# Kernel tuning notes

Hardware: AMD Instinct MI355X
Metric: run time of the kernel (lower is better)

## Reference

```python
import jax, jax.numpy as jnp
import numpy as np

N_NODES = 100000
N_EDGES = 3200000
IN_C, HID_C, OUT_C = 64, 64, 32


def setup_inputs() -> dict:
    key = jax.random.key(0)
    ks = jax.random.split(key, 8)
    x = jax.random.normal(ks[0], (N_NODES, IN_C), dtype=jnp.float32)
    edge_index = jax.random.randint(ks[1], (2, N_EDGES), 0, N_NODES, dtype=jnp.int64)
    s1 = 1.0 / np.sqrt(IN_C)
    s2 = 1.0 / np.sqrt(HID_C)
    W1l = jax.random.uniform(ks[2], (IN_C, HID_C), jnp.float32, -s1, s1)
    b1l = jnp.zeros((HID_C,), jnp.float32)
    W1r = jax.random.uniform(ks[3], (IN_C, HID_C), jnp.float32, -s1, s1)
    W2l = jax.random.uniform(ks[4], (HID_C, OUT_C), jnp.float32, -s2, s2)
    b2l = jnp.zeros((OUT_C,), jnp.float32)
    W2r = jax.random.uniform(ks[5], (HID_C, OUT_C), jnp.float32, -s2, s2)
    return {"x": x, "edge_index": edge_index, "W1l": W1l, "b1l": b1l,
            "W1r": W1r, "W2l": W2l, "b2l": b2l, "W2r": W2r}


def _sage_conv(x, src, dst, Wl, bl, Wr):
    # mean-aggregate source features onto destination nodes
    msg = x[src]                                              # [E, d] gather
    summed = jax.ops.segment_sum(msg, dst, num_segments=N_NODES)
    deg = jax.ops.segment_sum(jnp.ones((src.shape[0],), x.dtype), dst,
                              num_segments=N_NODES)
    agg = summed / jnp.maximum(deg, 1.0)[:, None]             # [N, d]
    return agg @ Wl + bl + x @ Wr                             # lin_l(agg)+lin_r(x)


def reference(x, edge_index, W1l, b1l, W1r, W2l, b2l, W2r):
    src, dst = edge_index[0], edge_index[1]
    h = jax.nn.relu(_sage_conv(x, src, dst, W1l, b1l, W1r))
    # dropout is identity in eval mode
    return _sage_conv(h, src, dst, W2l, b2l, W2r)
```

## Files before the change

kernel.cpp:

```cpp
#include <hip/hip_runtime.h>
#include <hip/hip_bf16.h>

#define N_NODES 100000
#define N_EDGES 3200000
#define NBKT 391
#define BKT_CAP 10240

typedef __hip_bfloat16 bf16;
typedef unsigned int uint;
typedef __attribute__((ext_vector_type(8))) short bf16x8;
typedef __attribute__((ext_vector_type(4))) float f32x4;

__device__ __forceinline__ float b2f(bf16 v) { return __bfloat162float(v); }

__device__ __forceinline__ float bits2f(unsigned short w) {
    union { unsigned short u; bf16 b; } c;
    c.u = w;
    return __bfloat162float(c.b);
}
__device__ __forceinline__ unsigned short f2bits(float f) {
    return (unsigned short)(__float_as_uint(f) >> 16);
}
__device__ __forceinline__ unsigned short f2bf_bits(float f) {
    bf16 b = __float2bfloat16(f);
    unsigned short u;
    __builtin_memcpy(&u, &b, 2);
    return u;
}

__device__ __forceinline__ int get_idx(const void* ei, long long pos, int is64) {
    if (is64) return (int)((const long long*)ei)[pos];
    return ((const int*)ei)[pos];
}
__device__ __forceinline__ float get_f(const void* p, long long pos, int isbf) {
    if (isbf) return b2f(((const bf16*)p)[pos]);
    return ((const float*)p)[pos];
}

__global__ void detect_kernel(const void* __restrict__ x,
                              const void* __restrict__ ei,
                              int* __restrict__ flags) {
    int lane = threadIdx.x;
    const unsigned short* xw = (const unsigned short*)x;
    float v = bits2f(xw[2 * lane]);
    bool plaus = (v == v) && fabsf(v) > 1e-3f && fabsf(v) < 1e2f;
    unsigned long long m1 = __ballot(plaus);
    const int* iw = (const int*)ei;
    bool z = (iw[2 * lane + 1] == 0);
    unsigned long long m2 = __ballot(z);
    if (lane == 0) {
        flags[0] = (__popcll(m1) >= 32) ? 1 : 0;
        flags[1] = (__popcll(m2) == 64) ? 1 : 0;
    }
}

__global__ __launch_bounds__(256) void scatterA_kernel(
    const void* __restrict__ ei, int* __restrict__ bucket_cursor,
    uint* __restrict__ bucket_data, const int* __restrict__ flags) {
    __shared__ int lhist[NBKT];
    __shared__ int lbase[NBKT];
    int is64 = flags[1];
    int t = threadIdx.x;
    int chunk0 = blockIdx.x * 8192;
    int dreg[32];

    for (int i = t; i < NBKT; i += 256) lhist[i] = 0;
    __syncthreads();
#pragma unroll
    for (int j = 0; j < 32; j++) {
        int e = chunk0 + j * 256 + t;
        int d = -1;
        if (e < N_EDGES) {
            d = get_idx(ei, (long long)N_EDGES + e, is64);
            atomicAdd(&lhist[d >> 8], 1);
        }
        dreg[j] = d;
    }
    __syncthreads();
    for (int i = t; i < NBKT; i += 256) {
        int c = lhist[i];
        lbase[i] = c ? atomicAdd(&bucket_cursor[i], c) : 0;
        lhist[i] = 0;
    }
    __syncthreads();
#pragma unroll
    for (int j = 0; j < 32; j++) {
        int e = chunk0 + j * 256 + t;
        int d = dreg[j];
        if (d >= 0) {
            int s = get_idx(ei, e, is64);
            int b = d >> 8;
            int o = lbase[b] + atomicAdd(&lhist[b], 1);
            if (o < BKT_CAP)
                bucket_data[(long long)b * BKT_CAP + o] = ((uint)(d & 255) << 17) | (uint)s;
        }
    }
}

__global__ void scanBuckets_kernel(const int* __restrict__ cnt,
                                   int* __restrict__ base) {
    __shared__ int buf[512];
    int t = threadIdx.x;
    int v = (t < NBKT) ? cnt[t] : 0;
    buf[t] = v;
    __syncthreads();
    for (int off = 1; off < 512; off <<= 1) {
        int add = (t >= off) ? buf[t - off] : 0;
        __syncthreads();
        buf[t] += add;
        __syncthreads();
    }
    if (t < NBKT) base[t] = buf[t] - v;
}

__global__ __launch_bounds__(256) void csrB_kernel(
    const int* __restrict__ bucket_cnt, const int* __restrict__ bucket_base,
    const uint* __restrict__ bucket_data, int* __restrict__ csr_src,
    int* __restrict__ row_start) {
    __shared__ int lh[256];
    __shared__ int buf[256];
    int b = blockIdx.x;
    int t = threadIdx.x;
    int cnt = bucket_cnt[b];
    if (cnt > BKT_CAP) cnt = BKT_CAP;
    int base = bucket_base[b];
    const uint* bd = bucket_data + (long long)b * BKT_CAP;

    lh[t] = 0;
    __syncthreads();
    for (int i = t; i < cnt; i += 256) atomicAdd(&lh[bd[i] >> 17], 1);
    __syncthreads();
    int v = lh[t];
    buf[t] = v;
    __syncthreads();
    for (int off = 1; off < 256; off <<= 1) {
        int add = (t >= off) ? buf[t - off] : 0;
        __syncthreads();
        buf[t] += add;
        __syncthreads();
    }
    int excl = buf[t] - v;
    int g = (b << 8) + t;
    if (g < N_NODES) row_start[g] = base + excl;
    lh[t] = excl;
    __syncthreads();
    for (int i = t; i < cnt; i += 256) {
        uint e = bd[i];
        int o = atomicAdd(&lh[e >> 17], 1);
        csr_src[base + o] = (int)(e & 0x1FFFFu);
    }
    if (b == 0 && t == 0) row_start[N_NODES] = N_EDGES;
}

__global__ __launch_bounds__(256) void gather1_kernel(
    const void* __restrict__ x, const int* __restrict__ row_start,
    const int* __restrict__ csr_src, bf16* __restrict__ aggbuf,
    const int* __restrict__ flags) {
    int isbf = flags[0];
    int t = threadIdx.x;
    int lane = t & 63;
    int gw = (blockIdx.x * 256 + t) >> 6;
    int nw = (gridDim.x * 256) >> 6;
    int e8 = lane >> 3, q8 = lane & 7;
    int e4 = lane >> 4, q16 = lane & 15;
    const uint4* xr4 = (const uint4*)x;

    for (int p = gw; p * 2 < N_NODES; p += nw) {
        int na = p * 2, nb = p * 2 + 1;
        int sa = row_start[na], ea = row_start[na + 1];
        int sb = row_start[nb], eb = row_start[nb + 1];
        int da = ea - sa, db = eb - sb;
        int maxd = max(da, db);
        float accA[8] = {0, 0, 0, 0, 0, 0, 0, 0};
        float accB[8] = {0, 0, 0, 0, 0, 0, 0, 0};
        float avA = 0.0f, avB = 0.0f;
        if (isbf) {
            for (int off = 0; off < maxd; off += 32) {
                int iA0 = sa + off + e8, iA1 = iA0 + 8, iA2 = iA0 + 16, iA3 = iA0 + 24;
                int iB0 = sb + off + e8, iB1 = iB0 + 8, iB2 = iB0 + 16, iB3 = iB0 + 24;
                int sA0 = (iA0 < ea) ? csr_src[iA0] : -1;
                int sA1 = (iA1 < ea) ? csr_src[iA1] : -1;
                int sA2 = (iA2 < ea) ? csr_src[iA2] : -1;
                int sA3 = (iA3 < ea) ? csr_src[iA3] : -1;
                int sB0 = (iB0 < eb) ? csr_src[iB0] : -1;
                int sB1 = (iB1 < eb) ? csr_src[iB1] : -1;
                int sB2 = (iB2 < eb) ? csr_src[iB2] : -1;
                int sB3 = (iB3 < eb) ? csr_src[iB3] : -1;
                uint4 vA0 = {0,0,0,0}, vA1 = {0,0,0,0}, vA2 = {0,0,0,0}, vA3 = {0,0,0,0};
                uint4 vB0 = {0,0,0,0}, vB1 = {0,0,0,0}, vB2 = {0,0,0,0}, vB3 = {0,0,0,0};
                if (sA0 >= 0) vA0 = xr4[sA0 * 8 + q8];
                if (sA1 >= 0) vA1 = xr4[sA1 * 8 + q8];
                if (sA2 >= 0) vA2 = xr4[sA2 * 8 + q8];
                if (sA3 >= 0) vA3 = xr4[sA3 * 8 + q8];
                if (sB0 >= 0) vB0 = xr4[sB0 * 8 + q8];
                if (sB1 >= 0) vB1 = xr4[sB1 * 8 + q8];
                if (sB2 >= 0) vB2 = xr4[sB2 * 8 + q8];
                if (sB3 >= 0) vB3 = xr4[sB3 * 8 + q8];
                accA[0] += __uint_as_float(vA0.x << 16) + __uint_as_float(vA1.x << 16)
                         + __uint_as_float(vA2.x << 16) + __uint_as_float(vA3.x << 16);
                accA[1] += __uint_as_float(vA0.x & 0xffff0000u) + __uint_as_float(vA1.x & 0xffff0000u)
                         + __uint_as_float(vA2.x & 0xffff0000u) + __uint_as_float(vA3.x & 0xffff0000u);
                accA[2] += __uint_as_float(vA0.y << 16) + __uint_as_float(vA1.y << 16)
                         + __uint_as_float(vA2.y << 16) + __uint_as_float(vA3.y << 16);
                accA[3] += __uint_as_float(vA0.y & 0xffff0000u) + __uint_as_float(vA1.y & 0xffff0000u)
                         + __uint_as_float(vA2.y & 0xffff0000u) + __uint_as_float(vA3.y & 0xffff0000u);
                accA[4] += __uint_as_float(vA0.z << 16) + __uint_as_float(vA1.z << 16)
                         + __uint_as_float(vA2.z << 16) + __uint_as_float(vA3.z << 16);
                accA[5] += __uint_as_float(vA0.z & 0xffff0000u) + __uint_as_float(vA1.z & 0xffff0000u)
                         + __uint_as_float(vA2.z & 0xffff0000u) + __uint_as_float(vA3.z & 0xffff0000u);
                accA[6] += __uint_as_float(vA0.w << 16) + __uint_as_float(vA1.w << 16)
                         + __uint_as_float(vA2.w << 16) + __uint_as_float(vA3.w << 16);
                accA[7] += __uint_as_float(vA0.w & 0xffff0000u) + __uint_as_float(vA1.w & 0xffff0000u)
                         + __uint_as_float(vA2.w & 0xffff0000u) + __uint_as_float(vA3.w & 0xffff0000u);
                accB[0] += __uint_as_float(vB0.x << 16) + __uint_as_float(vB1.x << 16)
                         + __uint_as_float(vB2.x << 16) + __uint_as_float(vB3.x << 16);
                accB[1] += __uint_as_float(vB0.x & 0xffff0000u) + __uint_as_float(vB1.x & 0xffff0000u)
                         + __uint_as_float(vB2.x & 0xffff0000u) + __uint_as_float(vB3.x & 0xffff0000u);
                accB[2] += __uint_as_float(vB0.y << 16) + __uint_as_float(vB1.y << 16)
                         + __uint_as_float(vB2.y << 16) + __uint_as_float(vB3.y << 16);
                accB[3] += __uint_as_float(vB0.y & 0xffff0000u) + __uint_as_float(vB1.y & 0xffff0000u)
                         + __uint_as_float(vB2.y & 0xffff0000u) + __uint_as_float(vB3.y & 0xffff0000u);
                accB[4] += __uint_as_float(vB0.z << 16) + __uint_as_float(vB1.z << 16)
                         + __uint_as_float(vB2.z << 16) + __uint_as_float(vB3.z << 16);
                accB[5] += __uint_as_float(vB0.z & 0xffff0000u) + __uint_as_float(vB1.z & 0xffff0000u)
                         + __uint_as_float(vB2.z & 0xffff0000u) + __uint_as_float(vB3.z & 0xffff0000u);
                accB[6] += __uint_as_float(vB0.w << 16) + __uint_as_float(vB1.w << 16)
                         + __uint_as_float(vB2.w << 16) + __uint_as_float(vB3.w << 16);
                accB[7] += __uint_as_float(vB0.w & 0xffff0000u) + __uint_as_float(vB1.w & 0xffff0000u)
                         + __uint_as_float(vB2.w & 0xffff0000u) + __uint_as_float(vB3.w & 0xffff0000u);
            }
#pragma unroll
            for (int mm = 8; mm <= 32; mm <<= 1)
#pragma unroll
                for (int k = 0; k < 8; k++) {
                    accA[k] += __shfl_xor(accA[k], mm, 64);
                    accB[k] += __shfl_xor(accB[k], mm, 64);
                }
#pragma unroll
            for (int k = 0; k < 8; k++) {
                float vA = __shfl(accA[k], lane >> 3, 64);
                float vB = __shfl(accB[k], lane >> 3, 64);
                avA = ((lane & 7) == k) ? vA : avA;
                avB = ((lane & 7) == k) ? vB : avB;
            }
        } else {
            const uint4* xf = (const uint4*)x;
            for (int off = 0; off < maxd; off += 16) {
                int iA0 = sa + off + e4, iA1 = iA0 + 4, iA2 = iA0 + 8, iA3 = iA0 + 12;
                int iB0 = sb + off + e4, iB1 = iB0 + 4, iB2 = iB0 + 8, iB3 = iB0 + 12;
                int sA0 = (iA0 < ea) ? csr_src[iA0] : -1;
                int sA1 = (iA1 < ea) ? csr_src[iA1] : -1;
                int sA2 = (iA2 < ea) ? csr_src[iA2] : -1;
                int sA3 = (iA3 < ea) ? csr_src[iA3] : -1;
                int sB0 = (iB0 < eb) ? csr_src[iB0] : -1;
                int sB1 = (iB1 < eb) ? csr_src[iB1] : -1;
                int sB2 = (iB2 < eb) ? csr_src[iB2] : -1;
                int sB3 = (iB3 < eb) ? csr_src[iB3] : -1;
                uint4 vA0 = {0,0,0,0}, vA1 = {0,0,0,0}, vA2 = {0,0,0,0}, vA3 = {0,0,0,0};
                uint4 vB0 = {0,0,0,0}, vB1 = {0,0,0,0}, vB2 = {0,0,0,0}, vB3 = {0,0,0,0};
                if (sA0 >= 0) vA0 = xf[sA0 * 16 + q16];
                if (sA1 >= 0) vA1 = xf[sA1 * 16 + q16];
                if (sA2 >= 0) vA2 = xf[sA2 * 16 + q16];
                if (sA3 >= 0) vA3 = xf[sA3 * 16 + q16];
                if (sB0 >= 0) vB0 = xf[sB0 * 16 + q16];
                if (sB1 >= 0) vB1 = xf[sB1 * 16 + q16];
                if (sB2 >= 0) vB2 = xf[sB2 * 16 + q16];
                if (sB3 >= 0) vB3 = xf[sB3 * 16 + q16];
                accA[0] += __uint_as_float(vA0.x) + __uint_as_float(vA1.x)
                         + __uint_as_float(vA2.x) + __uint_as_float(vA3.x);
                accA[1] += __uint_as_float(vA0.y) + __uint_as_float(vA1.y)
                         + __uint_as_float(vA2.y) + __uint_as_float(vA3.y);
                accA[2] += __uint_as_float(vA0.z) + __uint_as_float(vA1.z)
                         + __uint_as_float(vA2.z) + __uint_as_float(vA3.z);
                accA[3] += __uint_as_float(vA0.w) + __uint_as_float(vA1.w)
                         + __uint_as_float(vA2.w) + __uint_as_float(vA3.w);
                accB[0] += __uint_as_float(vB0.x) + __uint_as_float(vB1.x)
                         + __uint_as_float(vB2.x) + __uint_as_float(vB3.x);
                accB[1] += __uint_as_float(vB0.y) + __uint_as_float(vB1.y)
                         + __uint_as_float(vB2.y) + __uint_as_float(vB3.y);
                accB[2] += __uint_as_float(vB0.z) + __uint_as_float(vB1.z)
                         + __uint_as_float(vB2.z) + __uint_as_float(vB3.z);
                accB[3] += __uint_as_float(vB0.w) + __uint_as_float(vB1.w)
                         + __uint_as_float(vB2.w) + __uint_as_float(vB3.w);
            }
#pragma unroll
            for (int mm = 16; mm <= 32; mm <<= 1)
#pragma unroll
                for (int k = 0; k < 4; k++) {
                    accA[k] += __shfl_xor(accA[k], mm, 64);
                    accB[k] += __shfl_xor(accB[k], mm, 64);
                }
#pragma unroll
            for (int k = 0; k < 4; k++) {
                float vA = __shfl(accA[k], lane >> 2, 64);
                float vB = __shfl(accB[k], lane >> 2, 64);
                avA = ((lane & 3) == k) ? vA : avA;
                avB = ((lane & 3) == k) ? vB : avB;
            }
        }
        avA *= 1.0f / fmaxf((float)da, 1.0f);
        avB *= 1.0f / fmaxf((float)db, 1.0f);
        aggbuf[(long long)na * 64 + lane] = __float2bfloat16(avA);
        aggbuf[(long long)nb * 64 + lane] = __float2bfloat16(avB);
    }
}

__global__ __launch_bounds__(256) void gemm1_kernel(
    const void* __restrict__ x, const bf16* __restrict__ aggbuf,
    const void* __restrict__ W1l, const void* __restrict__ b1l,
    const void* __restrict__ W1r, const void* __restrict__ W2l,
    const void* __restrict__ b2l, const void* __restrict__ W2r,
    bf16* __restrict__ zbuf, bf16* __restrict__ rbuf,
    const int* __restrict__ flags) {
    __shared__ __align__(16) unsigned short sW1t[64][136];
    __shared__ __align__(16) unsigned short sA[64][136];
    __shared__ __align__(16) unsigned short sW2t[64][72];
    __shared__ __align__(16) unsigned short sH[64][72];
    __shared__ float sB1[64];
    __shared__ float sB2[32];

    int isbf = flags[0];
    int t = threadIdx.x;
    int n0 = blockIdx.x * 64;

    for (int i = t; i < 64 * 128; i += 256) {
        int n = i & 63, k = i >> 6;
        unsigned short v;
        if (isbf)
            v = (k < 64) ? ((const unsigned short*)W1l)[k * 64 + n]
                         : ((const unsigned short*)W1r)[(k - 64) * 64 + n];
        else
            v = f2bits((k < 64) ? ((const float*)W1l)[k * 64 + n]
                                : ((const float*)W1r)[(k - 64) * 64 + n]);
        sW1t[n][k] = v;
    }
    for (int i = t; i < 64 * 64; i += 256) {
        int n = i & 63, k = i >> 6;
        unsigned short v;
        if (isbf)
            v = (n < 32) ? ((const unsigned short*)W2l)[k * 32 + n]
                         : ((const unsigned short*)W2r)[k * 32 + (n - 32)];
        else
            v = f2bits((n < 32) ? ((const float*)W2l)[k * 32 + n]
                                : ((const float*)W2r)[k * 32 + (n - 32)]);
        sW2t[n][k] = v;
    }
    if (t < 64) sB1[t] = get_f(b1l, t, isbf);
    if (t < 32) sB2[t] = get_f(b2l, t, isbf);

    const uint4* ag4 = (const uint4*)aggbuf;
    if (isbf) {
        const uint4* x4 = (const uint4*)x;
        for (int i = t; i < 64 * 16; i += 256) {
            int m = i >> 4, c = i & 15;
            int nn = min(n0 + m, N_NODES - 1);
            uint4 v = (c < 8) ? ag4[(long long)nn * 8 + c]
                              : x4[(long long)nn * 8 + (c - 8)];
            *(uint4*)&sA[m][c * 8] = v;
        }
    } else {
        for (int i = t; i < 64 * 8; i += 256) {
            int m = i >> 3, c = i & 7;
            int nn = min(n0 + m, N_NODES - 1);
            *(uint4*)&sA[m][c * 8] = ag4[(long long)nn * 8 + c];
        }
        const float* xf = (const float*)x;
        for (int i = t; i < 64 * 64; i += 256) {
            int m = i >> 6, c = i & 63;
            int nn = min(n0 + m, N_NODES - 1);
            sA[m][64 + c] = f2bf_bits(xf[(long long)nn * 64 + c]);
        }
    }
    __syncthreads();

    int w = t >> 6, lane = t & 63;
    int mbase = w * 16;
    int q = lane >> 4, r15 = lane & 15;
    f32x4 acc1[4] = {{0,0,0,0},{0,0,0,0},{0,0,0,0},{0,0,0,0}};
#pragma unroll
    for (int ks = 0; ks < 4; ks++) {
        bf16x8 afrag = *(const bf16x8*)&sA[mbase + r15][ks * 32 + q * 8];
#pragma unroll
        for (int nt = 0; nt < 4; nt++) {
            bf16x8 bfrag = *(const bf16x8*)&sW1t[nt * 16 + r15][ks * 32 + q * 8];
            acc1[nt] = __builtin_amdgcn_mfma_f32_16x16x32_bf16(afrag, bfrag, acc1[nt], 0, 0, 0);
        }
    }
#pragma unroll
    for (int nt = 0; nt < 4; nt++) {
        int col = nt * 16 + r15;
        float bias = sB1[col];
#pragma unroll
        for (int rr = 0; rr < 4; rr++) {
            int m = mbase + q * 4 + rr;
            sH[m][col] = f2bf_bits(fmaxf(acc1[nt][rr] + bias, 0.0f));
        }
    }
    __syncthreads();

    f32x4 acc2[4] = {{0,0,0,0},{0,0,0,0},{0,0,0,0},{0,0,0,0}};
#pragma unroll
    for (int ks = 0; ks < 2; ks++) {
        bf16x8 afrag = *(const bf16x8*)&sH[mbase + r15][ks * 32 + q * 8];
#pragma unroll
        for (int nt = 0; nt < 4; nt++) {
            bf16x8 bfrag = *(const bf16x8*)&sW2t[nt * 16 + r15][ks * 32 + q * 8];
            acc2[nt] = __builtin_amdgcn_mfma_f32_16x16x32_bf16(afrag, bfrag, acc2[nt], 0, 0, 0);
        }
    }
#pragma unroll
    for (int nt = 0; nt < 4; nt++) {
        int col = nt * 16 + r15;
#pragma unroll
        for (int rr = 0; rr < 4; rr++) {
            int m = mbase + q * 4 + rr;
            int n = n0 + m;
            if (n < N_NODES) {
                float v = acc2[nt][rr];
                if (col < 32)
                    zbuf[(long long)n * 32 + col] = __float2bfloat16(v);
                else
                    rbuf[(long long)n * 32 + (col - 32)] = __float2bfloat16(v + sB2[col - 32]);
            }
        }
    }
}

__global__ void node2_kernel(const int* __restrict__ row_start,
                             const int* __restrict__ csr_src,
                             const bf16* __restrict__ z,
                             const bf16* __restrict__ rbuf,
                             void* __restrict__ out,
                             const int* __restrict__ flags) {
    int isbf = flags[0];
    int t = threadIdx.x;
    int lane = t & 63;
    int e = lane >> 2, q = lane & 3;
    int gw = (blockIdx.x * blockDim.x + t) >> 6;
    int nwaves = (gridDim.x * blockDim.x) >> 6;
    const uint4* zr = (const uint4*)z;

    for (int p = gw; p * 2 < N_NODES; p += nwaves) {
        int na = p * 2, nb = p * 2 + 1;
        int sa = row_start[na], ea = row_start[na + 1];
        int sb = row_start[nb], eb = row_start[nb + 1];
        float accA[8] = {0, 0, 0, 0, 0, 0, 0, 0};
        float accB[8] = {0, 0, 0, 0, 0, 0, 0, 0};
        int da = ea - sa, db = eb - sb;
        int maxd = max(da, db);
        for (int off = 0; off < maxd; off += 32) {
            int iA0 = sa + off + e, iA1 = iA0 + 16;
            int iB0 = sb + off + e, iB1 = iB0 + 16;
            int sA0 = (iA0 < ea) ? csr_src[iA0] : -1;
            int sA1 = (iA1 < ea) ? csr_src[iA1] : -1;
            int sB0 = (iB0 < eb) ? csr_src[iB0] : -1;
            int sB1 = (iB1 < eb) ? csr_src[iB1] : -1;
            uint4 vA0 = {0,0,0,0}, vA1 = {0,0,0,0}, vB0 = {0,0,0,0}, vB1 = {0,0,0,0};
            if (sA0 >= 0) vA0 = zr[sA0 * 4 + q];
            if (sA1 >= 0) vA1 = zr[sA1 * 4 + q];
            if (sB0 >= 0) vB0 = zr[sB0 * 4 + q];
            if (sB1 >= 0) vB1 = zr[sB1 * 4 + q];
            accA[0] += __uint_as_float(vA0.x << 16) + __uint_as_float(vA1.x << 16);
            accA[1] += __uint_as_float(vA0.x & 0xffff0000u) + __uint_as_float(vA1.x & 0xffff0000u);
            accA[2] += __uint_as_float(vA0.y << 16) + __uint_as_float(vA1.y << 16);
            accA[3] += __uint_as_float(vA0.y & 0xffff0000u) + __uint_as_float(vA1.y & 0xffff0000u);
            accA[4] += __uint_as_float(vA0.z << 16) + __uint_as_float(vA1.z << 16);
            accA[5] += __uint_as_float(vA0.z & 0xffff0000u) + __uint_as_float(vA1.z & 0xffff0000u);
            accA[6] += __uint_as_float(vA0.w << 16) + __uint_as_float(vA1.w << 16);
            accA[7] += __uint_as_float(vA0.w & 0xffff0000u) + __uint_as_float(vA1.w & 0xffff0000u);
            accB[0] += __uint_as_float(vB0.x << 16) + __uint_as_float(vB1.x << 16);
            accB[1] += __uint_as_float(vB0.x & 0xffff0000u) + __uint_as_float(vB1.x & 0xffff0000u);
            accB[2] += __uint_as_float(vB0.y << 16) + __uint_as_float(vB1.y << 16);
            accB[3] += __uint_as_float(vB0.y & 0xffff0000u) + __uint_as_float(vB1.y & 0xffff0000u);
            accB[4] += __uint_as_float(vB0.z << 16) + __uint_as_float(vB1.z << 16);
            accB[5] += __uint_as_float(vB0.z & 0xffff0000u) + __uint_as_float(vB1.z & 0xffff0000u);
            accB[6] += __uint_as_float(vB0.w << 16) + __uint_as_float(vB1.w << 16);
            accB[7] += __uint_as_float(vB0.w & 0xffff0000u) + __uint_as_float(vB1.w & 0xffff0000u);
        }
#pragma unroll
        for (int m = 4; m <= 32; m <<= 1)
#pragma unroll
            for (int k = 0; k < 8; k++) {
                accA[k] += __shfl_xor(accA[k], m, 64);
                accB[k] += __shfl_xor(accB[k], m, 64);
            }
        float svA = 0.0f, svB = 0.0f;
#pragma unroll
        for (int k = 0; k < 8; k++) {
            float vA = __shfl(accA[k], lane >> 3, 64);
            float vB = __shfl(accB[k], lane >> 3, 64);
            svA = ((lane & 7) == k) ? vA : svA;
            svB = ((lane & 7) == k) ? vB : svB;
        }
        if (lane < 32) {
            float invA = 1.0f / fmaxf((float)da, 1.0f);
            float invB = 1.0f / fmaxf((float)db, 1.0f);
            float valA = svA * invA + b2f(rbuf[(long long)na * 32 + lane]);
            float valB = svB * invB + b2f(rbuf[(long long)nb * 32 + lane]);
            if (isbf) {
                ((bf16*)out)[(long long)na * 32 + lane] = __float2bfloat16(valA);
                ((bf16*)out)[(long long)nb * 32 + lane] = __float2bfloat16(valB);
            } else {
                ((float*)out)[(long long)na * 32 + lane] = valA;
                ((float*)out)[(long long)nb * 32 + lane] = valB;
            }
        }
    }
}

extern "C" void kernel_launch(void* const* d_in, const int* in_sizes, int n_in,
                              void* d_out, int out_size, void* d_ws, size_t ws_size,
                              hipStream_t stream) {
    const void* x = d_in[0];
    const void* ei = d_in[1];
    const void* W1l = d_in[2];
    const void* b1l = d_in[3];
    const void* W1r = d_in[4];
    const void* W2l = d_in[5];
    const void* b2l = d_in[6];
    const void* W2r = d_in[7];

    char* ws = (char*)d_ws;
    uint* bucket_data = (uint*)ws;
    bf16* aggbuf = (bf16*)ws;
    int* csr_src = (int*)(ws + 16015424);
    int* row_start = (int*)(ws + 28815424);
    int* bucket_cursor = (int*)(ws + 29215488);
    int* bucket_base = (int*)(ws + 29217088);
    bf16* zbuf = (bf16*)(ws + 29218688);
    bf16* rbuf = (bf16*)(ws + 35618688);
    int* flags = (int*)(ws + 42018688);

    hipMemsetAsync(bucket_cursor, 0, NBKT * 4, stream);

    detect_kernel<<<1, 64, 0, stream>>>(x, ei, flags);
    scatterA_kernel<<<NBKT, 256, 0, stream>>>(ei, bucket_cursor, bucket_data, flags);
    scanBuckets_kernel<<<1, 512, 0, stream>>>(bucket_cursor, bucket_base);
    csrB_kernel<<<NBKT, 256, 0, stream>>>(bucket_cursor, bucket_base, bucket_data,
                                          csr_src, row_start);
    gather1_kernel<<<3125, 256, 0, stream>>>(x, row_start, csr_src, aggbuf, flags);
    gemm1_kernel<<<1563, 256, 0, stream>>>(x, aggbuf, W1l, b1l, W1r, W2l, b2l,
                                           W2r, zbuf, rbuf, flags);
    node2_kernel<<<8192, 256, 0, stream>>>(row_start, csr_src, zbuf, rbuf, d_out,
                                           flags);
}
```

Measured before the change: 355.9 us.

## Split gather feature channels across blocks and process four nodes per wave

```diff
diff --git a/kernel.cpp b/kernel.cpp
--- a/kernel.cpp
+++ b/kernel.cpp
@@ -152,6 +152,22 @@
     if (b == 0 && t == 0) row_start[N_NODES] = N_EDGES;
 }
 
+#define ACC8(acc, v, v2)                                                         \
+    acc[0] += __uint_as_float((v).x << 16) + __uint_as_float((v2).x << 16);       \
+    acc[1] += __uint_as_float((v).x & 0xffff0000u) + __uint_as_float((v2).x & 0xffff0000u); \
+    acc[2] += __uint_as_float((v).y << 16) + __uint_as_float((v2).y << 16);       \
+    acc[3] += __uint_as_float((v).y & 0xffff0000u) + __uint_as_float((v2).y & 0xffff0000u); \
+    acc[4] += __uint_as_float((v).z << 16) + __uint_as_float((v2).z << 16);       \
+    acc[5] += __uint_as_float((v).z & 0xffff0000u) + __uint_as_float((v2).z & 0xffff0000u); \
+    acc[6] += __uint_as_float((v).w << 16) + __uint_as_float((v2).w << 16);       \
+    acc[7] += __uint_as_float((v).w & 0xffff0000u) + __uint_as_float((v2).w & 0xffff0000u);
+
+#define ACCF4(acc, v, v2)                                                        \
+    acc[0] += __uint_as_float((v).x) + __uint_as_float((v2).x);                   \
+    acc[1] += __uint_as_float((v).y) + __uint_as_float((v2).y);                   \
+    acc[2] += __uint_as_float((v).z) + __uint_as_float((v2).z);                   \
+    acc[3] += __uint_as_float((v).w) + __uint_as_float((v2).w);
+
 __global__ __launch_bounds__(256) void gather1_kernel(
     const void* __restrict__ x, const int* __restrict__ row_start,
     const int* __restrict__ csr_src, bf16* __restrict__ aggbuf,
@@ -159,149 +175,151 @@
     int isbf = flags[0];
     int t = threadIdx.x;
     int lane = t & 63;
-    int gw = (blockIdx.x * 256 + t) >> 6;
-    int nw = (gridDim.x * 256) >> 6;
-    int e8 = lane >> 3, q8 = lane & 7;
-    int e4 = lane >> 4, q16 = lane & 15;
-    const uint4* xr4 = (const uint4*)x;
-
-    for (int p = gw; p * 2 < N_NODES; p += nw) {
-        int na = p * 2, nb = p * 2 + 1;
-        int sa = row_start[na], ea = row_start[na + 1];
-        int sb = row_start[nb], eb = row_start[nb + 1];
-        int da = ea - sa, db = eb - sb;
-        int maxd = max(da, db);
-        float accA[8] = {0, 0, 0, 0, 0, 0, 0, 0};
-        float accB[8] = {0, 0, 0, 0, 0, 0, 0, 0};
-        float avA = 0.0f, avB = 0.0f;
-        if (isbf) {
+    int w = t >> 6;
+    int bid = blockIdx.x;
+    int cz = (bid & 7) >> 1;
+    int wid = ((((bid >> 3) << 1) | (bid & 1)) << 2) + w;
+    int nw = gridDim.x;
+    const uint4* x4 = (const uint4*)x;
+
+    if (isbf) {
+        int e32 = lane >> 1, q2 = lane & 1;
+        int cbase = cz * 2 + q2;
+        for (int quad = wid; quad < N_NODES / 4; quad += nw) {
+            int nb0 = quad * 4;
+            int r0 = row_start[nb0], r1 = row_start[nb0 + 1],
+                r2 = row_start[nb0 + 2], r3 = row_start[nb0 + 3],
+                r4 = row_start[nb0 + 4];
+            int d0 = r1 - r0, d1 = r2 - r1, d2 = r3 - r2, d3 = r4 - r3;
+            int maxd = max(max(d0, d1), max(d2, d3));
+            float a0[8] = {0,0,0,0,0,0,0,0}, a1[8] = {0,0,0,0,0,0,0,0};
+            float a2[8] = {0,0,0,0,0,0,0,0}, a3[8] = {0,0,0,0,0,0,0,0};
+            for (int off = 0; off < maxd; off += 64) {
+                int iA = r0 + off + e32, iA2 = iA + 32;
+                int iB = r1 + off + e32, iB2 = iB + 32;
+                int iC = r2 + off + e32, iC2 = iC + 32;
+                int iD = r3 + off + e32, iD2 = iD + 32;
+                int sA  = (iA  < r1) ? csr_src[iA]  : -1;
+                int sA2 = (iA2 < r1) ? csr_src[iA2] : -1;
+                int sB  = (iB  < r2) ? csr_src[iB]  : -1;
+                int sB2 = (iB2 < r2) ? csr_src[iB2] : -1;
+                int sC  = (iC  < r3) ? csr_src[iC]  : -1;
+                int sC2 = (iC2 < r3) ? csr_src[iC2] : -1;
+                int sD  = (iD  < r4) ? csr_src[iD]  : -1;
+                int sD2 = (iD2 < r4) ? csr_src[iD2] : -1;
+                uint4 vA = {0,0,0,0}, vA2 = {0,0,0,0}, vB = {0,0,0,0}, vB2 = {0,0,0,0};
+                uint4 vC = {0,0,0,0}, vC2 = {0,0,0,0}, vD = {0,0,0,0}, vD2 = {0,0,0,0};
+                if (sA  >= 0) vA  = x4[sA  * 8 + cbase];
+                if (sA2 >= 0) vA2 = x4[sA2 * 8 + cbase];
+                if (sB  >= 0) vB  = x4[sB  * 8 + cbase];
+                if (sB2 >= 0) vB2 = x4[sB2 * 8 + cbase];
+                if (sC  >= 0) vC  = x4[sC  * 8 + cbase];
+                if (sC2 >= 0) vC2 = x4[sC2 * 8 + cbase];
+                if (sD  >= 0) vD  = x4[sD  * 8 + cbase];
+                if (sD2 >= 0) vD2 = x4[sD2 * 8 + cbase];
+                ACC8(a0, vA, vA2)
+                ACC8(a1, vB, vB2)
+                ACC8(a2, vC, vC2)
+                ACC8(a3, vD, vD2)
+            }
+#pragma unroll
+            for (int m = 2; m <= 32; m <<= 1)
+#pragma unroll
+                for (int k = 0; k < 8; k++) {
+                    a0[k] += __shfl_xor(a0[k], m, 64);
+                    a1[k] += __shfl_xor(a1[k], m, 64);
+                    a2[k] += __shfl_xor(a2[k], m, 64);
+                    a3[k] += __shfl_xor(a3[k], m, 64);
+                }
+            int c = lane & 15, nl = lane >> 4;
+            int srcq = (lane >> 3) & 1;
+            float v0 = 0, v1 = 0, v2 = 0, v3 = 0;
+#pragma unroll
+            for (int k = 0; k < 8; k++) {
+                float t0 = __shfl(a0[k], srcq, 64);
+                float t1 = __shfl(a1[k], srcq, 64);
+                float t2 = __shfl(a2[k], srcq, 64);
+                float t3 = __shfl(a3[k], srcq, 64);
+                bool sel = (lane & 7) == k;
+                v0 = sel ? t0 : v0;
+                v1 = sel ? t1 : v1;
+                v2 = sel ? t2 : v2;
+                v3 = sel ? t3 : v3;
+            }
+            float val = (nl == 0) ? v0 : (nl == 1) ? v1 : (nl == 2) ? v2 : v3;
+            int dd = (nl == 0) ? d0 : (nl == 1) ? d1 : (nl == 2) ? d2 : d3;
+            val *= 1.0f / fmaxf((float)dd, 1.0f);
+            aggbuf[(long long)(nb0 + nl) * 64 + cz * 16 + c] = __float2bfloat16(val);
+        }
+    } else {
+        int e16 = lane >> 2, q4 = lane & 3;
+        int cbase = cz * 4 + q4;
+        for (int quad = wid; quad < N_NODES / 4; quad += nw) {
+            int nb0 = quad * 4;
+            int r0 = row_start[nb0], r1 = row_start[nb0 + 1],
+                r2 = row_start[nb0 + 2], r3 = row_start[nb0 + 3],
+                r4 = row_start[nb0 + 4];
+            int d0 = r1 - r0, d1 = r2 - r1, d2 = r3 - r2, d3 = r4 - r3;
+            int maxd = max(max(d0, d1), max(d2, d3));
+            float a0[4] = {0,0,0,0}, a1[4] = {0,0,0,0};
+            float a2[4] = {0,0,0,0}, a3[4] = {0,0,0,0};
             for (int off = 0; off < maxd; off += 32) {
-                int iA0 = sa + off + e8, iA1 = iA0 + 8, iA2 = iA0 + 16, iA3 = iA0 + 24;
-                int iB0 = sb + off + e8, iB1 = iB0 + 8, iB2 = iB0 + 16, iB3 = iB0 + 24;
-                int sA0 = (iA0 < ea) ? csr_src[iA0] : -1;
-                int sA1 = (iA1 < ea) ? csr_src[iA1] : -1;
-                int sA2 = (iA2 < ea) ? csr_src[iA2] : -1;
-                int sA3 = (iA3 < ea) ? csr_src[iA3] : -1;
-                int sB0 = (iB0 < eb) ? csr_src[iB0] : -1;
-                int sB1 = (iB1 < eb) ? csr_src[iB1] : -1;
-                int sB2 = (iB2 < eb) ? csr_src[iB2] : -1;
-                int sB3 = (iB3 < eb) ? csr_src[iB3] : -1;
-                uint4 vA0 = {0,0,0,0}, vA1 = {0,0,0,0}, vA2 = {0,0,0,0}, vA3 = {0,0,0,0};
-                uint4 vB0 = {0,0,0,0}, vB1 = {0,0,0,0}, vB2 = {0,0,0,0}, vB3 = {0,0,0,0};
-                if (sA0 >= 0) vA0 = xr4[sA0 * 8 + q8];
-                if (sA1 >= 0) vA1 = xr4[sA1 * 8 + q8];
-                if (sA2 >= 0) vA2 = xr4[sA2 * 8 + q8];
-                if (sA3 >= 0) vA3 = xr4[sA3 * 8 + q8];
-                if (sB0 >= 0) vB0 = xr4[sB0 * 8 + q8];
-                if (sB1 >= 0) vB1 = xr4[sB1 * 8 + q8];
-                if (sB2 >= 0) vB2 = xr4[sB2 * 8 + q8];
-                if (sB3 >= 0) vB3 = xr4[sB3 * 8 + q8];
-                accA[0] += __uint_as_float(vA0.x << 16) + __uint_as_float(vA1.x << 16)
-                         + __uint_as_float(vA2.x << 16) + __uint_as_float(vA3.x << 16);
-                accA[1] += __uint_as_float(vA0.x & 0xffff0000u) + __uint_as_float(vA1.x & 0xffff0000u)
-                         + __uint_as_float(vA2.x & 0xffff0000u) + __uint_as_float(vA3.x & 0xffff0000u);
-                accA[2] += __uint_as_float(vA0.y << 16) + __uint_as_float(vA1.y << 16)
-                         + __uint_as_float(vA2.y << 16) + __uint_as_float(vA3.y << 16);
-                accA[3] += __uint_as_float(vA0.y & 0xffff0000u) + __uint_as_float(vA1.y & 0xffff0000u)
-                         + __uint_as_float(vA2.y & 0xffff0000u) + __uint_as_float(vA3.y & 0xffff0000u);
-                accA[4] += __uint_as_float(vA0.z << 16) + __uint_as_float(vA1.z << 16)
-                         + __uint_as_float(vA2.z << 16) + __uint_as_float(vA3.z << 16);
-                accA[5] += __uint_as_float(vA0.z & 0xffff0000u) + __uint_as_float(vA1.z & 0xffff0000u)
-                         + __uint_as_float(vA2.z & 0xffff0000u) + __uint_as_float(vA3.z & 0xffff0000u);
-                accA[6] += __uint_as_float(vA0.w << 16) + __uint_as_float(vA1.w << 16)
-                         + __uint_as_float(vA2.w << 16) + __uint_as_float(vA3.w << 16);
-                accA[7] += __uint_as_float(vA0.w & 0xffff0000u) + __uint_as_float(vA1.w & 0xffff0000u)
-                         + __uint_as_float(vA2.w & 0xffff0000u) + __uint_as_float(vA3.w & 0xffff0000u);
-                accB[0] += __uint_as_float(vB0.x << 16) + __uint_as_float(vB1.x << 16)
-                         + __uint_as_float(vB2.x << 16) + __uint_as_float(vB3.x << 16);
-                accB[1] += __uint_as_float(vB0.x & 0xffff0000u) + __uint_as_float(vB1.x & 0xffff0000u)
-                         + __uint_as_float(vB2.x & 0xffff0000u) + __uint_as_float(vB3.x & 0xffff0000u);
-                accB[2] += __uint_as_float(vB0.y << 16) + __uint_as_float(vB1.y << 16)
-                         + __uint_as_float(vB2.y << 16) + __uint_as_float(vB3.y << 16);
-                accB[3] += __uint_as_float(vB0.y & 0xffff0000u) + __uint_as_float(vB1.y & 0xffff0000u)
-                         + __uint_as_float(vB2.y & 0xffff0000u) + __uint_as_float(vB3.y & 0xffff0000u);
-                accB[4] += __uint_as_float(vB0.z << 16) + __uint_as_float(vB1.z << 16)
-                         + __uint_as_float(vB2.z << 16) + __uint_as_float(vB3.z << 16);
-                accB[5] += __uint_as_float(vB0.z & 0xffff0000u) + __uint_as_float(vB1.z & 0xffff0000u)
-                         + __uint_as_float(vB2.z & 0xffff0000u) + __uint_as_float(vB3.z & 0xffff0000u);
-                accB[6] += __uint_as_float(vB0.w << 16) + __uint_as_float(vB1.w << 16)
-                         + __uint_as_float(vB2.w << 16) + __uint_as_float(vB3.w << 16);
-                accB[7] += __uint_as_float(vB0.w & 0xffff0000u) + __uint_as_float(vB1.w & 0xffff0000u)
-                         + __uint_as_float(vB2.w & 0xffff0000u) + __uint_as_float(vB3.w & 0xffff0000u);
+                int iA = r0 + off + e16, iA2 = iA + 16;
+                int iB = r1 + off + e16, iB2 = iB + 16;
+                int iC = r2 + off + e16, iC2 = iC + 16;
+                int iD = r3 + off + e16, iD2 = iD + 16;
+                int sA  = (iA  < r1) ? csr_src[iA]  : -1;
+                int sA2 = (iA2 < r1) ? csr_src[iA2] : -1;
+                int sB  = (iB  < r2) ? csr_src[iB]  : -1;
+                int sB2 = (iB2 < r2) ? csr_src[iB2] : -1;
+                int sC  = (iC  < r3) ? csr_src[iC]  : -1;
+                int sC2 = (iC2 < r3) ? csr_src[iC2] : -1;
+                int sD  = (iD  < r4) ? csr_src[iD]  : -1;
+                int sD2 = (iD2 < r4) ? csr_src[iD2] : -1;
+                uint4 vA = {0,0,0,0}, vA2 = {0,0,0,0}, vB = {0,0,0,0}, vB2 = {0,0,0,0};
+                uint4 vC = {0,0,0,0}, vC2 = {0,0,0,0}, vD = {0,0,0,0}, vD2 = {0,0,0,0};
+                if (sA  >= 0) vA  = x4[sA  * 16 + cbase];
+                if (sA2 >= 0) vA2 = x4[sA2 * 16 + cbase];
+                if (sB  >= 0) vB  = x4[sB  * 16 + cbase];
+                if (sB2 >= 0) vB2 = x4[sB2 * 16 + cbase];
+                if (sC  >= 0) vC  = x4[sC  * 16 + cbase];
+                if (sC2 >= 0) vC2 = x4[sC2 * 16 + cbase];
+                if (sD  >= 0) vD  = x4[sD  * 16 + cbase];
+                if (sD2 >= 0) vD2 = x4[sD2 * 16 + cbase];
+                ACCF4(a0, vA, vA2)
+                ACCF4(a1, vB, vB2)
+                ACCF4(a2, vC, vC2)
+                ACCF4(a3, vD, vD2)
             }
 #pragma unroll
-            for (int mm = 8; mm <= 32; mm <<= 1)
-#pragma unroll
-                for (int k = 0; k < 8; k++) {
-                    accA[k] += __shfl_xor(accA[k], mm, 64);
-                    accB[k] += __shfl_xor(accB[k], mm, 64);
+            for (int m = 4; m <= 32; m <<= 1)
+#pragma unroll
+                for (int k = 0; k < 4; k++) {
+                    a0[k] += __shfl_xor(a0[k], m, 64);
+                    a1[k] += __shfl_xor(a1[k], m, 64);
+                    a2[k] += __shfl_xor(a2[k], m, 64);
+                    a3[k] += __shfl_xor(a3[k], m, 64);
                 }
-#pragma unroll
-            for (int k = 0; k < 8; k++) {
-                float vA = __shfl(accA[k], lane >> 3, 64);
-                float vB = __shfl(accB[k], lane >> 3, 64);
-                avA = ((lane & 7) == k) ? vA : avA;
-                avB = ((lane & 7) == k) ? vB : avB;
+            int c = lane & 15, nl = lane >> 4;
+            int srcq = (lane >> 2) & 3;
+            float v0 = 0, v1 = 0, v2 = 0, v3 = 0;
+#pragma unroll
+            for (int k = 0; k < 4; k++) {
+                float t0 = __shfl(a0[k], srcq, 64);
+                float t1 = __shfl(a1[k], srcq, 64);
+                float t2 = __shfl(a2[k], srcq, 64);
+                float t3 = __shfl(a3[k], srcq, 64);
+                bool sel = (lane & 3) == k;
+                v0 = sel ? t0 : v0;
+                v1 = sel ? t1 : v1;
+                v2 = sel ? t2 : v2;
+                v3 = sel ? t3 : v3;
             }
-        } else {
-            const uint4* xf = (const uint4*)x;
-            for (int off = 0; off < maxd; off += 16) {
-                int iA0 = sa + off + e4, iA1 = iA0 + 4, iA2 = iA0 + 8, iA3 = iA0 + 12;
-                int iB0 = sb + off + e4, iB1 = iB0 + 4, iB2 = iB0 + 8, iB3 = iB0 + 12;
-                int sA0 = (iA0 < ea) ? csr_src[iA0] : -1;
-                int sA1 = (iA1 < ea) ? csr_src[iA1] : -1;
-                int sA2 = (iA2 < ea) ? csr_src[iA2] : -1;
-                int sA3 = (iA3 < ea) ? csr_src[iA3] : -1;
-                int sB0 = (iB0 < eb) ? csr_src[iB0] : -1;
-                int sB1 = (iB1 < eb) ? csr_src[iB1] : -1;
-                int sB2 = (iB2 < eb) ? csr_src[iB2] : -1;
-                int sB3 = (iB3 < eb) ? csr_src[iB3] : -1;
-                uint4 vA0 = {0,0,0,0}, vA1 = {0,0,0,0}, vA2 = {0,0,0,0}, vA3 = {0,0,0,0};
-                uint4 vB0 = {0,0,0,0}, vB1 = {0,0,0,0}, vB2 = {0,0,0,0}, vB3 = {0,0,0,0};
-                if (sA0 >= 0) vA0 = xf[sA0 * 16 + q16];
-                if (sA1 >= 0) vA1 = xf[sA1 * 16 + q16];
-                if (sA2 >= 0) vA2 = xf[sA2 * 16 + q16];
-                if (sA3 >= 0) vA3 = xf[sA3 * 16 + q16];
-                if (sB0 >= 0) vB0 = xf[sB0 * 16 + q16];
-                if (sB1 >= 0) vB1 = xf[sB1 * 16 + q16];
-                if (sB2 >= 0) vB2 = xf[sB2 * 16 + q16];
-                if (sB3 >= 0) vB3 = xf[sB3 * 16 + q16];
-                accA[0] += __uint_as_float(vA0.x) + __uint_as_float(vA1.x)
-                         + __uint_as_float(vA2.x) + __uint_as_float(vA3.x);
-                accA[1] += __uint_as_float(vA0.y) + __uint_as_float(vA1.y)
-                         + __uint_as_float(vA2.y) + __uint_as_float(vA3.y);
-                accA[2] += __uint_as_float(vA0.z) + __uint_as_float(vA1.z)
-                         + __uint_as_float(vA2.z) + __uint_as_float(vA3.z);
-                accA[3] += __uint_as_float(vA0.w) + __uint_as_float(vA1.w)
-                         + __uint_as_float(vA2.w) + __uint_as_float(vA3.w);
-                accB[0] += __uint_as_float(vB0.x) + __uint_as_float(vB1.x)
-                         + __uint_as_float(vB2.x) + __uint_as_float(vB3.x);
-                accB[1] += __uint_as_float(vB0.y) + __uint_as_float(vB1.y)
-                         + __uint_as_float(vB2.y) + __uint_as_float(vB3.y);
-                accB[2] += __uint_as_float(vB0.z) + __uint_as_float(vB1.z)
-                         + __uint_as_float(vB2.z) + __uint_as_float(vB3.z);
-                accB[3] += __uint_as_float(vB0.w) + __uint_as_float(vB1.w)
-                         + __uint_as_float(vB2.w) + __uint_as_float(vB3.w);
-            }
-#pragma unroll
-            for (int mm = 16; mm <= 32; mm <<= 1)
-#pragma unroll
-                for (int k = 0; k < 4; k++) {
-                    accA[k] += __shfl_xor(accA[k], mm, 64);
-                    accB[k] += __shfl_xor(accB[k], mm, 64);
-                }
-#pragma unroll
-            for (int k = 0; k < 4; k++) {
-                float vA = __shfl(accA[k], lane >> 2, 64);
-                float vB = __shfl(accB[k], lane >> 2, 64);
-                avA = ((lane & 3) == k) ? vA : avA;
-                avB = ((lane & 3) == k) ? vB : avB;
-            }
-        }
-        avA *= 1.0f / fmaxf((float)da, 1.0f);
-        avB *= 1.0f / fmaxf((float)db, 1.0f);
-        aggbuf[(long long)na * 64 + lane] = __float2bfloat16(avA);
-        aggbuf[(long long)nb * 64 + lane] = __float2bfloat16(avB);
+            float val = (nl == 0) ? v0 : (nl == 1) ? v1 : (nl == 2) ? v2 : v3;
+            int dd = (nl == 0) ? d0 : (nl == 1) ? d1 : (nl == 2) ? d2 : d3;
+            val *= 1.0f / fmaxf((float)dd, 1.0f);
+            aggbuf[(long long)(nb0 + nl) * 64 + cz * 16 + c] = __float2bfloat16(val);
+        }
     }
 }
 
@@ -426,85 +444,93 @@
     }
 }
 
-__global__ void node2_kernel(const int* __restrict__ row_start,
-                             const int* __restrict__ csr_src,
-                             const bf16* __restrict__ z,
-                             const bf16* __restrict__ rbuf,
-                             void* __restrict__ out,
-                             const int* __restrict__ flags) {
+__global__ __launch_bounds__(256) void node2_kernel(
+    const int* __restrict__ row_start, const int* __restrict__ csr_src,
+    const bf16* __restrict__ z, const bf16* __restrict__ rbuf,
+    void* __restrict__ out, const int* __restrict__ flags) {
     int isbf = flags[0];
     int t = threadIdx.x;
     int lane = t & 63;
-    int e = lane >> 2, q = lane & 3;
-    int gw = (blockIdx.x * blockDim.x + t) >> 6;
-    int nwaves = (gridDim.x * blockDim.x) >> 6;
+    int w = t >> 6;
+    int bid = blockIdx.x;
+    int cz = (bid & 7) >> 2;
+    int wid = ((((bid >> 3) << 2) | (bid & 3)) << 2) + w;
+    int nw = gridDim.x * 2;
     const uint4* zr = (const uint4*)z;
 
-    for (int p = gw; p * 2 < N_NODES; p += nwaves) {
-        int na = p * 2, nb = p * 2 + 1;
-        int sa = row_start[na], ea = row_start[na + 1];
-        int sb = row_start[nb], eb = row_start[nb + 1];
-        float accA[8] = {0, 0, 0, 0, 0, 0, 0, 0};
-        float accB[8] = {0, 0, 0, 0, 0, 0, 0, 0};
-        int da = ea - sa, db = eb - sb;
-        int maxd = max(da, db);
-        for (int off = 0; off < maxd; off += 32) {
-            int iA0 = sa + off + e, iA1 = iA0 + 16;
-            int iB0 = sb + off + e, iB1 = iB0 + 16;
-            int sA0 = (iA0 < ea) ? csr_src[iA0] : -1;
-            int sA1 = (iA1 < ea) ? csr_src[iA1] : -1;
-            int sB0 = (iB0 < eb) ? csr_src[iB0] : -1;
-            int sB1 = (iB1 < eb) ? csr_src[iB1] : -1;
-            uint4 vA0 = {0,0,0,0}, vA1 = {0,0,0,0}, vB0 = {0,0,0,0}, vB1 = {0,0,0,0};
-            if (sA0 >= 0) vA0 = zr[sA0 * 4 + q];
-            if (sA1 >= 0) vA1 = zr[sA1 * 4 + q];
-            if (sB0 >= 0) vB0 = zr[sB0 * 4 + q];
-            if (sB1 >= 0) vB1 = zr[sB1 * 4 + q];
-            accA[0] += __uint_as_float(vA0.x << 16) + __uint_as_float(vA1.x << 16);
-            accA[1] += __uint_as_float(vA0.x & 0xffff0000u) + __uint_as_float(vA1.x & 0xffff0000u);
-            accA[2] += __uint_as_float(vA0.y << 16) + __uint_as_float(vA1.y << 16);
-            accA[3] += __uint_as_float(vA0.y & 0xffff0000u) + __uint_as_float(vA1.y & 0xffff0000u);
-            accA[4] += __uint_as_float(vA0.z << 16) + __uint_as_float(vA1.z << 16);
-            accA[5] += __uint_as_float(vA0.z & 0xffff0000u) + __uint_as_float(vA1.z & 0xffff0000u);
-            accA[6] += __uint_as_float(vA0.w << 16) + __uint_as_float(vA1.w << 16);
-            accA[7] += __uint_as_float(vA0.w & 0xffff0000u) + __uint_as_float(vA1.w & 0xffff0000u);
-            accB[0] += __uint_as_float(vB0.x << 16) + __uint_as_float(vB1.x << 16);
-            accB[1] += __uint_as_float(vB0.x & 0xffff0000u) + __uint_as_float(vB1.x & 0xffff0000u);
-            accB[2] += __uint_as_float(vB0.y << 16) + __uint_as_float(vB1.y << 16);
-            accB[3] += __uint_as_float(vB0.y & 0xffff0000u) + __uint_as_float(vB1.y & 0xffff0000u);
-            accB[4] += __uint_as_float(vB0.z << 16) + __uint_as_float(vB1.z << 16);
-            accB[5] += __uint_as_float(vB0.z & 0xffff0000u) + __uint_as_float(vB1.z & 0xffff0000u);
-            accB[6] += __uint_as_float(vB0.w << 16) + __uint_as_float(vB1.w << 16);
-            accB[7] += __uint_as_float(vB0.w & 0xffff0000u) + __uint_as_float(vB1.w & 0xffff0000u);
-        }
-#pragma unroll
-        for (int m = 4; m <= 32; m <<= 1)
+    int e32 = lane >> 1, q2 = lane & 1;
+    int cbase = cz * 2 + q2;
+    for (int quad = wid; quad < N_NODES / 4; quad += nw) {
+        int nb0 = quad * 4;
+        int r0 = row_start[nb0], r1 = row_start[nb0 + 1],
+            r2 = row_start[nb0 + 2], r3 = row_start[nb0 + 3],
+            r4 = row_start[nb0 + 4];
+        int d0 = r1 - r0, d1 = r2 - r1, d2 = r3 - r2, d3 = r4 - r3;
+        int maxd = max(max(d0, d1), max(d2, d3));
+        float a0[8] = {0,0,0,0,0,0,0,0}, a1[8] = {0,0,0,0,0,0,0,0};
+        float a2[8] = {0,0,0,0,0,0,0,0}, a3[8] = {0,0,0,0,0,0,0,0};
+        for (int off = 0; off < maxd; off += 64) {
+            int iA = r0 + off + e32, iA2 = iA + 32;
+            int iB = r1 + off + e32, iB2 = iB + 32;
+            int iC = r2 + off + e32, iC2 = iC + 32;
+            int iD = r3 + off + e32, iD2 = iD + 32;
+            int sA  = (iA  < r1) ? csr_src[iA]  : -1;
+            int sA2 = (iA2 < r1) ? csr_src[iA2] : -1;
+            int sB  = (iB  < r2) ? csr_src[iB]  : -1;
+            int sB2 = (iB2 < r2) ? csr_src[iB2] : -1;
+            int sC  = (iC  < r3) ? csr_src[iC]  : -1;
+            int sC2 = (iC2 < r3) ? csr_src[iC2] : -1;
+            int sD  = (iD  < r4) ? csr_src[iD]  : -1;
+            int sD2 = (iD2 < r4) ? csr_src[iD2] : -1;
+            uint4 vA = {0,0,0,0}, vA2 = {0,0,0,0}, vB = {0,0,0,0}, vB2 = {0,0,0,0};
+            uint4 vC = {0,0,0,0}, vC2 = {0,0,0,0}, vD = {0,0,0,0}, vD2 = {0,0,0,0};
+            if (sA  >= 0) vA  = zr[sA  * 4 + cbase];
+            if (sA2 >= 0) vA2 = zr[sA2 * 4 + cbase];
+            if (sB  >= 0) vB  = zr[sB  * 4 + cbase];
+            if (sB2 >= 0) vB2 = zr[sB2 * 4 + cbase];
+            if (sC  >= 0) vC  = zr[sC  * 4 + cbase];
+            if (sC2 >= 0) vC2 = zr[sC2 * 4 + cbase];
+            if (sD  >= 0) vD  = zr[sD  * 4 + cbase];
+            if (sD2 >= 0) vD2 = zr[sD2 * 4 + cbase];
+            ACC8(a0, vA, vA2)
+            ACC8(a1, vB, vB2)
+            ACC8(a2, vC, vC2)
+            ACC8(a3, vD, vD2)
+        }
+#pragma unroll
+        for (int m = 2; m <= 32; m <<= 1)
 #pragma unroll
             for (int k = 0; k < 8; k++) {
-                accA[k] += __shfl_xor(accA[k], m, 64);
-                accB[k] += __shfl_xor(accB[k], m, 64);
+                a0[k] += __shfl_xor(a0[k], m, 64);
+                a1[k] += __shfl_xor(a1[k], m, 64);
+                a2[k] += __shfl_xor(a2[k], m, 64);
+                a3[k] += __shfl_xor(a3[k], m, 64);
             }
-        float svA = 0.0f, svB = 0.0f;
+        int c = lane & 15, nl = lane >> 4;
+        int srcq = (lane >> 3) & 1;
+        float v0 = 0, v1 = 0, v2 = 0, v3 = 0;
 #pragma unroll
         for (int k = 0; k < 8; k++) {
-            float vA = __shfl(accA[k], lane >> 3, 64);
-            float vB = __shfl(accB[k], lane >> 3, 64);
-            svA = ((lane & 7) == k) ? vA : svA;
-            svB = ((lane & 7) == k) ? vB : svB;
-        }
-        if (lane < 32) {
-            float invA = 1.0f / fmaxf((float)da, 1.0f);
-            float invB = 1.0f / fmaxf((float)db, 1.0f);
-            float valA = svA * invA + b2f(rbuf[(long long)na * 32 + lane]);
-            float valB = svB * invB + b2f(rbuf[(long long)nb * 32 + lane]);
-            if (isbf) {
-                ((bf16*)out)[(long long)na * 32 + lane] = __float2bfloat16(valA);
-                ((bf16*)out)[(long long)nb * 32 + lane] = __float2bfloat16(valB);
-            } else {
-                ((float*)out)[(long long)na * 32 + lane] = valA;
-                ((float*)out)[(long long)nb * 32 + lane] = valB;
-            }
-        }
+            float t0 = __shfl(a0[k], srcq, 64);
+            float t1 = __shfl(a1[k], srcq, 64);
+            float t2 = __shfl(a2[k], srcq, 64);
+            float t3 = __shfl(a3[k], srcq, 64);
+            bool sel = (lane & 7) == k;
+            v0 = sel ? t0 : v0;
+            v1 = sel ? t1 : v1;
+            v2 = sel ? t2 : v2;
+            v3 = sel ? t3 : v3;
+        }
+        float val = (nl == 0) ? v0 : (nl == 1) ? v1 : (nl == 2) ? v2 : v3;
+        int dd = (nl == 0) ? d0 : (nl == 1) ? d1 : (nl == 2) ? d2 : d3;
+        int n = nb0 + nl;
+        int ch = cz * 16 + c;
+        float res = val * (1.0f / fmaxf((float)dd, 1.0f))
+                  + b2f(rbuf[(long long)n * 32 + ch]);
+        if (isbf)
+            ((bf16*)out)[(long long)n * 32 + ch] = __float2bfloat16(res);
+        else
+            ((float*)out)[(long long)n * 32 + ch] = res;
     }
 }
 
@@ -538,9 +564,9 @@
     scanBuckets_kernel<<<1, 512, 0, stream>>>(bucket_cursor, bucket_base);
     csrB_kernel<<<NBKT, 256, 0, stream>>>(bucket_cursor, bucket_base, bucket_data,
                                           csr_src, row_start);
-    gather1_kernel<<<3125, 256, 0, stream>>>(x, row_start, csr_src, aggbuf, flags);
+    gather1_kernel<<<4096, 256, 0, stream>>>(x, row_start, csr_src, aggbuf, flags);
     gemm1_kernel<<<1563, 256, 0, stream>>>(x, aggbuf, W1l, b1l, W1r, W2l, b2l,
                                            W2r, zbuf, rbuf, flags);
-    node2_kernel<<<8192, 256, 0, stream>>>(row_start, csr_src, zbuf, rbuf, d_out,
+    node2_kernel<<<4096, 256, 0, stream>>>(row_start, csr_src, zbuf, rbuf, d_out,
                                            flags);
 }
```

Measured after the change: 486.5 us. 36.7% more time.
